# Optimization experiments

Hardware: AMD Instinct MI355X
Metric: run time of the kernel (lower is better)

## Reference

```python
import jax, jax.numpy as jnp
import numpy as np

P_SCALAR = 40.0
NEG_INF = -1e9


def setup_inputs() -> dict:
    key = jax.random.key(0)
    ks = jax.random.split(key, 6)
    B, Dk, Dv, T, H, W = 2, 128, 512, 2, 64, 64
    qkey = jax.random.normal(ks[0], (B, Dk, H, W), dtype=jnp.float32)
    qval = jax.random.normal(ks[1], (B, Dv, H, W), dtype=jnp.float32)
    mkey = jax.random.normal(ks[2], (B, Dk, T, H, W), dtype=jnp.float32)
    mval = jax.random.normal(ks[3], (B, Dv, T, H, W), dtype=jnp.float32)
    qmask = jax.random.bernoulli(ks[4], 0.5, (B, 1, H, W))
    mmask = jax.random.bernoulli(ks[5], 0.5, (B, 1, T, H, W))
    return {"qkey": qkey, "qval": qval, "qmask": qmask,
            "mkey": mkey, "mval": mval, "mmask": mmask}


def reference(qkey, qval, qmask, mkey, mval, mmask):
    # Faithful vectorized version of maskRead: for each batch, attention from
    # masked query pixels over masked memory pixels, scatter back into zeros.
    # Boolean-gather + softmax over gathered rows == full softmax with masked
    # logits set to -inf (rows outside mmask get zero probability).
    B, Dk, H, W = qkey.shape
    Dv = qval.shape[1]
    qk = qkey.reshape(B, Dk, H * W)            # [B, Dk, Nq]
    mk = mkey.reshape(B, Dk, -1)               # [B, Dk, Nm]
    mv = mval.reshape(B, Dv, -1)               # [B, Dv, Nm]
    qm = qmask.reshape(B, H * W)               # [B, Nq]
    mm = mmask.reshape(B, -1)                  # [B, Nm]

    # p[b, m, q] = <mk[b,:,m], qk[b,:,q]> * p_scalar, softmax over m
    p = jnp.einsum('bdm,bdq->bmq', mk, qk) * P_SCALAR
    p = jnp.where(mm[:, :, None], p, NEG_INF)
    p = jax.nn.softmax(p, axis=1)              # [B, Nm, Nq]

    read = jnp.einsum('bvm,bmq->bvq', mv, p)   # [B, Dv, Nq]

    # zero out query pixels outside qmask; skip batches with empty masks
    valid = qm[:, None, :] & mm.any(axis=1)[:, None, None] & qm.any(axis=1)[:, None, None]
    qread = jnp.where(valid, read, 0.0)
    return qread.reshape(B, Dv, H, W)
```

## Files before the change

kernel.cpp:

```cpp
#include <hip/hip_runtime.h>

#define NQ 4096
#define NM 8192
#define DK 128
#define DV 512
#define BATCH 2
#define NT (NM / 64)
#define KTS 8192
#define VTILE 16384

typedef __attribute__((ext_vector_type(8))) short short8;
typedef __attribute__((ext_vector_type(4))) float f32x4;
typedef unsigned short ushort_t;

#define MF(A_, B_, C_) __builtin_amdgcn_mfma_f32_16x16x32_bf16(A_, B_, C_, 0, 0, 0)

static __device__ __forceinline__ unsigned short f2bf(float x) {
    union { float f; unsigned int u; } c; c.f = x;
    unsigned int u = c.u;
    return (unsigned short)((u + 0x7FFFu + ((u >> 16) & 1u)) >> 16);
}
static __device__ __forceinline__ float bf2f(unsigned short h) {
    union { unsigned int u; float f; } c; c.u = ((unsigned int)h) << 16;
    return c.f;
}

static __device__ __forceinline__ size_t vaddr(int b, int pos, int dv) {
    const int mt = pos >> 6, m64 = pos & 63;
    const int dvh = dv >> 8, rr = dv & 255;
    return (((size_t)(b * NT + mt) * 2 + dvh) * VTILE)
         + (rr >> 6) * 4096 + ((rr >> 4) & 3) * 1024
         + (m64 >> 5) * 512
         + ((((m64 >> 4) & 1) * 2 + ((m64 >> 3) & 1)) * 128)
         + (rr & 15) * 8 + (m64 & 7);
}

#define LOADK(AH, AL, itn_) do {                                              \
    const size_t ktb_ = kbase + (size_t)(itn_) * KTS;                         \
    _Pragma("unroll")                                                         \
    for (int ks_ = 0; ks_ < 4; ++ks_) {                                       \
        AH[ks_] = *(const short8*)(kh0 + ktb_ + ks_ * 512);                   \
        AL[ks_] = *(const short8*)(kl0 + ktb_ + ks_ * 512);                   \
    }                                                                         \
} while (0)

__global__ __launch_bounds__(1024) void scan_kernel(
    const int* __restrict__ qmask, const int* __restrict__ mmask,
    int* __restrict__ cidx, int* __restrict__ cpos,
    int* __restrict__ cnts, int* __restrict__ qflags) {
    const int b = blockIdx.x;
    const int t = threadIdx.x;
    const int lane = t & 63;
    const int w = t >> 6;
    __shared__ int wsum[16];
    __shared__ int qsh;

    const int* mp = mmask + b * NM;
    const int base = t * 8;
    int val[8];
#pragma unroll
    for (int i = 0; i < 8; ++i) val[i] = (mp[base + i] != 0);
    int c0 = 0;
#pragma unroll
    for (int i = 0; i < 8; ++i) c0 += val[i];

    int c = c0;
#pragma unroll
    for (int off = 1; off < 64; off <<= 1) {
        int n = __shfl_up(c, off, 64);
        if (lane >= off) c += n;
    }
    if (lane == 63) wsum[w] = c;
    if (t == 0) qsh = 0;
    __syncthreads();
    if (t == 0) {
        int s = 0;
#pragma unroll
        for (int i = 0; i < 16; ++i) { s += wsum[i]; wsum[i] = s; }
    }
    __syncthreads();
    const int wbase = (w == 0) ? 0 : wsum[w - 1];
    int run = wbase + (c - c0);
#pragma unroll
    for (int i = 0; i < 8; ++i) {
        int m = base + i;
        cpos[b * NM + m] = run;
        if (val[i]) { cidx[b * NM + run] = m; ++run; }
    }

    int qa = 0;
    for (int i = t; i < NQ; i += 1024) qa |= (qmask[b * NQ + i] != 0);
    if (qa) atomicOr(&qsh, 1);
    __syncthreads();
    if (t == 0) { cnts[b] = wsum[15]; qflags[b] = qsh; }
}

__global__ __launch_bounds__(256) void prep_all_kernel(
    const float* __restrict__ qkey, const float* __restrict__ mkey,
    const float* __restrict__ mval, const int* __restrict__ mmask,
    const int* __restrict__ cpos, const int* __restrict__ cnts,
    ushort_t* __restrict__ Qhi, ushort_t* __restrict__ Qlo,
    ushort_t* __restrict__ Khi, ushort_t* __restrict__ Klo,
    ushort_t* __restrict__ Vc) {
    __shared__ float t32[32][33];
    const int g = blockIdx.x;

    if (g < 1024) {
        const int bx = g & 127, by = (g >> 7) & 3, b = g >> 9;
        const int d0 = by * 32, n0 = bx * 32;
        for (int l = threadIdx.x; l < 1024; l += 256) {
            int r = l >> 5, c = l & 31;
            t32[r][c] = qkey[((size_t)b * DK + d0 + r) * NQ + n0 + c];
        }
        __syncthreads();
        for (int l = threadIdx.x; l < 1024; l += 256) {
            int r = l >> 5, c = l & 31;
            float f = t32[c][r];
            unsigned short h = f2bf(f);
            unsigned short lw = f2bf(f - bf2f(h));
            size_t off = ((size_t)b * NQ + n0 + r) * DK + d0 + c;
            Qhi[off] = h;
            Qlo[off] = lw;
        }
        return;
    }
    if (g < 3072) {
        const int h0 = g - 1024;
        const int bx = h0 & 255, by = (h0 >> 8) & 3, b = h0 >> 10;
        const int d0 = by * 32, n0 = bx * 32;
        for (int l = threadIdx.x; l < 1024; l += 256) {
            int r = l >> 5, c = l & 31;
            t32[r][c] = mkey[((size_t)b * DK + d0 + r) * NM + n0 + c];
        }
        __syncthreads();
        for (int l = threadIdx.x; l < 1024; l += 256) {
            int r = l >> 5, c = l & 31;
            int m = n0 + r;
            if (mmask[b * NM + m] != 0) {
                int pos = cpos[b * NM + m];
                float f = t32[c][r];
                unsigned short hh = f2bf(f);
                unsigned short lw = f2bf(f - bf2f(hh));
                int d = d0 + c;
                size_t off = ((size_t)(b * NT + (pos >> 6))) * KTS
                           + ((pos >> 4) & 3) * 2048 + (d >> 5) * 512
                           + ((d >> 3) & 3) * 128 + (pos & 15) * 8 + (d & 7);
                Khi[off] = hh;
                Klo[off] = lw;
            }
        }
        return;
    }
    const int h0 = g - 3072;
    const int bx = h0 & 63;
    const int by = (h0 >> 6) % 9;
    const int b = h0 / 576;
    const int dv0 = bx * 8;
    if (by == 8) {
        const int cnt = cnts[b];
        const int pend = ((cnt + 63) >> 6) * 64;
        const int dv = dv0 + (threadIdx.x >> 5);
        for (int p = cnt + (threadIdx.x & 31); p < pend; p += 32)
            Vc[vaddr(b, p, dv)] = 0;
        return;
    }
    const int m = by * 1024 + threadIdx.x * 4;
    const int4 mm = *(const int4*)(mmask + b * NM + m);
    const int4 cp = *(const int4*)(cpos + b * NM + m);
#pragma unroll
    for (int i = 0; i < 8; ++i) {
        const int dv = dv0 + i;
        const float4 v = *(const float4*)(mval + ((size_t)b * DV + dv) * NM + m);
        if (mm.x) Vc[vaddr(b, cp.x, dv)] = f2bf(v.x);
        if (mm.y) Vc[vaddr(b, cp.y, dv)] = f2bf(v.y);
        if (mm.z) Vc[vaddr(b, cp.z, dv)] = f2bf(v.z);
        if (mm.w) Vc[vaddr(b, cp.w, dv)] = f2bf(v.w);
    }
}

__global__ __launch_bounds__(256, 3) void stats_kernel(
    const ushort_t* __restrict__ Qhi, const ushort_t* __restrict__ Khi,
    const int* __restrict__ cnts, float* __restrict__ mpart) {
    const int t = threadIdx.x;
    const int lane = t & 63;
    const int w = t >> 6;
    const int quad = lane >> 4;
    const int col = lane & 15;
    const int bid = blockIdx.x;
    const int part = bid & 3;
    const int b = (bid >> 2) & 1;
    const int qb = (bid >> 3) * 64;

    const int cnt = cnts[b];
    const int nit = (cnt + 63) >> 6;
    const int it0 = (nit * part) >> 2;
    const int it1 = (nit * (part + 1)) >> 2;

    __shared__ float red_m[4][64];

    short8 qfh[4][4];
    {
        const ushort_t* qhp = Qhi + ((size_t)b * NQ + qb) * DK;
#pragma unroll
        for (int qt = 0; qt < 4; ++qt)
#pragma unroll
            for (int ks = 0; ks < 4; ++ks)
                qfh[qt][ks] = *(const short8*)(qhp + (size_t)(qt * 16 + col) * DK + ks * 32 + quad * 8);
    }

    const f32x4 zero4 = {0.f, 0.f, 0.f, 0.f};
    float mloc[4] = {-3.0e38f, -3.0e38f, -3.0e38f, -3.0e38f};
    const ushort_t* kh0 = Khi + w * 2048 + lane * 8;
    const size_t kbase = (size_t)(b * NT) * KTS;

#define LOADKH(A_, itn_) do {                                                 \
    const size_t ktb_ = kbase + (size_t)(itn_) * KTS;                         \
    _Pragma("unroll")                                                         \
    for (int ks_ = 0; ks_ < 4; ++ks_)                                         \
        A_[ks_] = *(const short8*)(kh0 + ktb_ + ks_ * 512);                   \
} while (0)

#define STPH(CK, NK, it_, itn_) do {                                          \
    LOADKH(NK, itn_);                                                         \
    f32x4 aS[4];                                                              \
    _Pragma("unroll")                                                         \
    for (int qt = 0; qt < 4; ++qt) aS[qt] = zero4;                            \
    _Pragma("unroll")                                                         \
    for (int ks = 0; ks < 4; ++ks)                                            \
        _Pragma("unroll")                                                     \
        for (int qt = 0; qt < 4; ++qt)                                        \
            aS[qt] = MF(CK[ks], qfh[qt][ks], aS[qt]);                         \
    const int mrow_ = (it_) * 64 + w * 16 + quad * 4;                         \
    _Pragma("unroll")                                                         \
    for (int r = 0; r < 4; ++r) {                                             \
        if (mrow_ + r < cnt) {                                                \
            _Pragma("unroll")                                                 \
            for (int qt = 0; qt < 4; ++qt)                                    \
                mloc[qt] = fmaxf(mloc[qt], aS[qt][r] * 40.0f);                \
        }                                                                     \
    }                                                                         \
} while (0)

    short8 kA[4], kB[4];
    int it = it0;
    if (it < it1) {
        LOADKH(kA, it);
        int itn;
        while (true) {
            itn = (it + 1 < it1) ? it + 1 : it;
            STPH(kA, kB, it, itn);
            if (++it >= it1) break;
            itn = (it + 1 < it1) ? it + 1 : it;
            STPH(kB, kA, it, itn);
            if (++it >= it1) break;
        }
    }
#undef STPH
#undef LOADKH

#pragma unroll
    for (int qt = 0; qt < 4; ++qt) {
        float m = mloc[qt];
        m = fmaxf(m, __shfl_xor(m, 16, 64));
        m = fmaxf(m, __shfl_xor(m, 32, 64));
        if (lane < 16) red_m[w][qt * 16 + col] = m;
    }
    __syncthreads();
    if (t < 64) {
        float M = -3.0e38f;
#pragma unroll
        for (int ww = 0; ww < 4; ++ww) M = fmaxf(M, red_m[ww][t]);
        mpart[((size_t)(b * 4 + part)) * NQ + qb + t] = M;
    }
}

__global__ __launch_bounds__(256, 3) void pv_kernel(
    const ushort_t* __restrict__ Qhi, const ushort_t* __restrict__ Qlo,
    const ushort_t* __restrict__ Khi, const ushort_t* __restrict__ Klo,
    const ushort_t* __restrict__ Vimg, const int* __restrict__ cnts,
    const float* __restrict__ mpart, float* __restrict__ out0,
    float* __restrict__ out1, float* __restrict__ out2,
    float* __restrict__ lsum) {
    const int t = threadIdx.x;
    const int lane = t & 63;
    const int w = t >> 6;
    const int quad = lane >> 4;
    const int col = lane & 15;
    const int bid = blockIdx.x;
    const int b = bid & 1;
    const int dvh = (bid >> 1) & 1;
    const int r3 = bid >> 2;
    const int chunk = r3 % 3;
    const int qb = (r3 / 3) * 64;

    const int cnt = cnts[b];
    const int nit = (cnt + 63) >> 6;
    const int it0 = (nit * chunk) / 3;
    const int it1 = (nit * (chunk + 1)) / 3;

    __shared__ __align__(16) ushort_t Q_s[2][4][4][512];
    __shared__ __align__(16) ushort_t P_s[2][64][68];

    float gm[4];
#pragma unroll
    for (int qt = 0; qt < 4; ++qt) {
        float M = -3.0e38f;
#pragma unroll
        for (int c = 0; c < 4; ++c)
            M = fmaxf(M, mpart[((size_t)(b * 4 + c)) * NQ + qb + qt * 16 + col]);
        gm[qt] = M + 8.0f;
    }

    {
        const int r = t >> 2, ks4 = t & 3;
        const int qt_ = r >> 4, col_ = r & 15;
        const ushort_t* qhp = Qhi + ((size_t)b * NQ + qb + r) * DK + ks4 * 32;
        const ushort_t* qlp = Qlo + ((size_t)b * NQ + qb + r) * DK + ks4 * 32;
#pragma unroll
        for (int qd = 0; qd < 4; ++qd) {
            *(short8*)&Q_s[0][qt_][ks4][qd * 128 + col_ * 8] = *(const short8*)(qhp + qd * 8);
            *(short8*)&Q_s[1][qt_][ks4][qd * 128 + col_ * 8] = *(const short8*)(qlp + qd * 8);
        }
    }
    __syncthreads();

    const ushort_t* kh0 = Khi + w * 2048 + lane * 8;
    const ushort_t* kl0 = Klo + w * 2048 + lane * 8;
    const size_t kbase = (size_t)(b * NT) * KTS;
    const ushort_t* vl0 = Vimg + ((size_t)(b * NT) * 2 + dvh) * VTILE
                        + w * 4096 + lane * 8;

    const f32x4 zero4 = {0.f, 0.f, 0.f, 0.f};
    const short8 vones = {(short)0x3F80, (short)0x3F80, (short)0x3F80,
                          (short)0x3F80, (short)0x3F80, (short)0x3F80,
                          (short)0x3F80, (short)0x3F80};
    const bool doL = (dvh == 0) && (w == 0);
    f32x4 accO[4][4];
#pragma unroll
    for (int vt = 0; vt < 4; ++vt)
#pragma unroll
        for (int qt = 0; qt < 4; ++qt) accO[vt][qt] = zero4;
    f32x4 accL[4];
#pragma unroll
    for (int qt = 0; qt < 4; ++qt) accL[qt] = zero4;

    for (int it = it0; it < it1; ++it) {
        const int pb = (it - it0) & 1;
        short8 kh[4], kl[4];
        LOADK(kh, kl, it);
        f32x4 aS[4];
#pragma unroll
        for (int qt = 0; qt < 4; ++qt) aS[qt] = zero4;
#pragma unroll
        for (int qt = 0; qt < 4; ++qt) {
#pragma unroll
            for (int ks = 0; ks < 4; ++ks) {
                const short8 qh = *(const short8*)&Q_s[0][qt][ks][lane * 8];
                const short8 ql = *(const short8*)&Q_s[1][qt][ks][lane * 8];
                aS[qt] = MF(kh[ks], qh, aS[qt]);
                aS[qt] = MF(kh[ks], ql, aS[qt]);
                aS[qt] = MF(kl[ks], qh, aS[qt]);
            }
        }
        const ushort_t* vp = vl0 + (size_t)it * (2 * VTILE);
        short8 vf[4][2];
#pragma unroll
        for (int vt = 0; vt < 4; ++vt) {
            vf[vt][0] = *(const short8*)(vp + vt * 1024);
            vf[vt][1] = *(const short8*)(vp + vt * 1024 + 512);
        }
        const int mrow = it * 64 + w * 16 + quad * 4;
#pragma unroll
        for (int qt = 0; qt < 4; ++qt) {
            float p[4];
#pragma unroll
            for (int r = 0; r < 4; ++r)
                p[r] = (mrow + r < cnt) ? __expf(aS[qt][r] * 40.0f - gm[qt]) : 0.0f;
            ushort4 pk;
            pk.x = f2bf(p[0]); pk.y = f2bf(p[1]);
            pk.z = f2bf(p[2]); pk.w = f2bf(p[3]);
            *(ushort4*)&P_s[pb][qt * 16 + col][w * 16 + quad * 4] = pk;
        }
        asm volatile("s_waitcnt lgkmcnt(0)" ::: "memory");
        __builtin_amdgcn_s_barrier();
        __builtin_amdgcn_sched_barrier(0);
#pragma unroll
        for (int k2 = 0; k2 < 2; ++k2) {
            short8 pq[4];
#pragma unroll
            for (int qt = 0; qt < 4; ++qt)
                pq[qt] = *(const short8*)&P_s[pb][qt * 16 + col][k2 * 32 + quad * 8];
#pragma unroll
            for (int vt = 0; vt < 4; ++vt)
#pragma unroll
                for (int qt = 0; qt < 4; ++qt)
                    accO[vt][qt] = MF(vf[vt][k2], pq[qt], accO[vt][qt]);
            if (doL) {
#pragma unroll
                for (int qt = 0; qt < 4; ++qt)
                    accL[qt] = MF(vones, pq[qt], accL[qt]);
            }
        }
    }

    float* pbase = (chunk == 0) ? out0 : ((chunk == 1) ? out1 : out2);
#pragma unroll
    for (int qt = 0; qt < 4; ++qt) {
        const int q = qb + qt * 16 + col;
#pragma unroll
        for (int vt = 0; vt < 4; ++vt)
#pragma unroll
            for (int r = 0; r < 4; ++r) {
                int dv = dvh * 256 + w * 64 + vt * 16 + quad * 4 + r;
                pbase[((size_t)b * DV + dv) * NQ + q] = accO[vt][qt][r];
            }
    }
    if (doL && lane < 16) {
#pragma unroll
        for (int qt = 0; qt < 4; ++qt)
            lsum[((size_t)(b * 3 + chunk)) * NQ + qb + qt * 16 + col] = accL[qt][0];
    }
}

__global__ __launch_bounds__(256) void combine_kernel(
    const float* p0, const float* __restrict__ p1,
    const float* __restrict__ p2, const float* __restrict__ lsum,
    const int* __restrict__ cnts, const int* __restrict__ qflags,
    const int* __restrict__ qmask, float* out) {
    const size_t i = ((size_t)blockIdx.x * 256 + threadIdx.x) * 4;
    const int b = (int)(i >> 21);
    const int q = (int)(i & (NQ - 1));
    f32x4 a = *(const f32x4*)(p0 + i);
    f32x4 c = *(const f32x4*)(p1 + i);
    f32x4 d = *(const f32x4*)(p2 + i);
    f32x4 l0 = *(const f32x4*)(lsum + (size_t)(b * 3) * NQ + q);
    f32x4 l1 = *(const f32x4*)(lsum + (size_t)(b * 3 + 1) * NQ + q);
    f32x4 l2 = *(const f32x4*)(lsum + (size_t)(b * 3 + 2) * NQ + q);
    const int4 qm = *(const int4*)(qmask + b * NQ + q);
    const bool bv = (qflags[b] != 0) && (cnts[b] > 0);
    f32x4 r;
    float lv;
    lv = l0[0] + l1[0] + l2[0]; r[0] = (bv && qm.x && lv > 0.f) ? (a[0] + c[0] + d[0]) / lv : 0.f;
    lv = l0[1] + l1[1] + l2[1]; r[1] = (bv && qm.y && lv > 0.f) ? (a[1] + c[1] + d[1]) / lv : 0.f;
    lv = l0[2] + l1[2] + l2[2]; r[2] = (bv && qm.z && lv > 0.f) ? (a[2] + c[2] + d[2]) / lv : 0.f;
    lv = l0[3] + l1[3] + l2[3]; r[3] = (bv && qm.w && lv > 0.f) ? (a[3] + c[3] + d[3]) / lv : 0.f;
    *(f32x4*)(out + i) = r;
}

extern "C" void kernel_launch(void* const* d_in, const int* in_sizes, int n_in,
                              void* d_out, int out_size, void* d_ws, size_t ws_size,
                              hipStream_t stream) {
    const float* qkey  = (const float*)d_in[0];
    const int*   qmask = (const int*)d_in[2];
    const float* mkey  = (const float*)d_in[3];
    const float* mval  = (const float*)d_in[4];
    const int*   mmask = (const int*)d_in[5];
    float* out = (float*)d_out;

    char* ws = (char*)d_ws;
    size_t off = 0;
    const size_t QS  = (size_t)BATCH * NQ * DK * 2;
    const size_t KS2 = (size_t)BATCH * NM * DK * 2;
    const size_t VS  = (size_t)BATCH * NT * 2 * VTILE * 2;
    const size_t OS  = (size_t)BATCH * DV * NQ * 4;
    ushort_t* Qhi = (ushort_t*)(ws + off); off += QS;
    ushort_t* Qlo = (ushort_t*)(ws + off); off += QS;
    ushort_t* Khi = (ushort_t*)(ws + off); off += KS2;
    ushort_t* Klo = (ushort_t*)(ws + off); off += KS2;
    ushort_t* Vc  = (ushort_t*)(ws + off); off += VS;
    float* part1  = (float*)(ws + off); off += OS;
    float* part2  = (float*)(ws + off); off += OS;
    float* mpart  = (float*)(ws + off); off += (size_t)BATCH * 4 * NQ * 4;
    float* lsum   = (float*)(ws + off); off += (size_t)BATCH * 3 * NQ * 4;
    int* cidx     = (int*)(ws + off); off += (size_t)BATCH * NM * 4;
    int* cpos     = (int*)(ws + off); off += (size_t)BATCH * NM * 4;
    int* cnts     = (int*)(ws + off); off += 64;
    int* qflags   = (int*)(ws + off); off += 64;

    scan_kernel<<<BATCH, 1024, 0, stream>>>(qmask, mmask, cidx, cpos, cnts, qflags);

    prep_all_kernel<<<4224, 256, 0, stream>>>(
        qkey, mkey, mval, mmask, cpos, cnts, Qhi, Qlo, Khi, Klo, Vc);

    stats_kernel<<<(NQ / 64) * 8, 256, 0, stream>>>(Qhi, Khi, cnts, mpart);

    pv_kernel<<<(NQ / 64) * 12, 256, 0, stream>>>(
        Qhi, Qlo, Khi, Klo, Vc, cnts, mpart, out, part1, part2, lsum);

    combine_kernel<<<(int)((size_t)BATCH * DV * NQ / 1024), 256, 0, stream>>>(
        out, part1, part2, lsum, cnts, qflags, qmask, out);
}
```

Before: 233.9 us.

## Store split-K partial outputs in fp16, split prep kernel, add MFMA priority hints

The three split-K partial output buffers are now stored as fp16 instead of fp32, and all three go to the workspace instead of one aliasing the output. This halves the partial-result write and read traffic between pv_kernel and combine_kernel. The prep kernel is split into a Q/K conversion kernel and a separate V compaction kernel with a 3D grid. s_setprio is raised around the MFMA loops in pv_kernel. Rounding unnormalized partial sums to fp16 adds precision error and could overflow if the partial sums exceed the fp16 range.

Measured after the change: 221.6 us. 1.06x faster.

```diff
diff --git a/kernel.cpp b/kernel.cpp
--- a/kernel.cpp
+++ b/kernel.cpp
@@ -1,4 +1,5 @@
 #include <hip/hip_runtime.h>
+#include <hip/hip_fp16.h>
 
 #define NQ 4096
 #define NM 8192
@@ -23,6 +24,14 @@
 static __device__ __forceinline__ float bf2f(unsigned short h) {
     union { unsigned int u; float f; } c; c.u = ((unsigned int)h) << 16;
     return c.f;
+}
+static __device__ __forceinline__ ushort_t f2h(float x) {
+    __half h = __float2half(x);
+    return *(ushort_t*)&h;
+}
+static __device__ __forceinline__ float h2f(ushort_t u) {
+    __half h = *(__half*)&u;
+    return __half2float(h);
 }
 
 static __device__ __forceinline__ size_t vaddr(int b, int pos, int dv) {
@@ -95,13 +104,11 @@
     if (t == 0) { cnts[b] = wsum[15]; qflags[b] = qsh; }
 }
 
-__global__ __launch_bounds__(256) void prep_all_kernel(
+__global__ __launch_bounds__(256) void prep_qk_kernel(
     const float* __restrict__ qkey, const float* __restrict__ mkey,
-    const float* __restrict__ mval, const int* __restrict__ mmask,
-    const int* __restrict__ cpos, const int* __restrict__ cnts,
+    const int* __restrict__ mmask, const int* __restrict__ cpos,
     ushort_t* __restrict__ Qhi, ushort_t* __restrict__ Qlo,
-    ushort_t* __restrict__ Khi, ushort_t* __restrict__ Klo,
-    ushort_t* __restrict__ Vc) {
+    ushort_t* __restrict__ Khi, ushort_t* __restrict__ Klo) {
     __shared__ float t32[32][33];
     const int g = blockIdx.x;
 
@@ -124,57 +131,57 @@
         }
         return;
     }
-    if (g < 3072) {
-        const int h0 = g - 1024;
-        const int bx = h0 & 255, by = (h0 >> 8) & 3, b = h0 >> 10;
-        const int d0 = by * 32, n0 = bx * 32;
-        for (int l = threadIdx.x; l < 1024; l += 256) {
-            int r = l >> 5, c = l & 31;
-            t32[r][c] = mkey[((size_t)b * DK + d0 + r) * NM + n0 + c];
-        }
-        __syncthreads();
-        for (int l = threadIdx.x; l < 1024; l += 256) {
-            int r = l >> 5, c = l & 31;
-            int m = n0 + r;
-            if (mmask[b * NM + m] != 0) {
-                int pos = cpos[b * NM + m];
-                float f = t32[c][r];
-                unsigned short hh = f2bf(f);
-                unsigned short lw = f2bf(f - bf2f(hh));
-                int d = d0 + c;
-                size_t off = ((size_t)(b * NT + (pos >> 6))) * KTS
-                           + ((pos >> 4) & 3) * 2048 + (d >> 5) * 512
-                           + ((d >> 3) & 3) * 128 + (pos & 15) * 8 + (d & 7);
-                Khi[off] = hh;
-                Klo[off] = lw;
-            }
-        }
-        return;
-    }
-    const int h0 = g - 3072;
-    const int bx = h0 & 63;
-    const int by = (h0 >> 6) % 9;
-    const int b = h0 / 576;
-    const int dv0 = bx * 8;
-    if (by == 8) {
+    const int h0 = g - 1024;
+    const int bx = h0 & 255, by = (h0 >> 8) & 3, b = h0 >> 10;
+    const int d0 = by * 32, n0 = bx * 32;
+    for (int l = threadIdx.x; l < 1024; l += 256) {
+        int r = l >> 5, c = l & 31;
+        t32[r][c] = mkey[((size_t)b * DK + d0 + r) * NM + n0 + c];
+    }
+    __syncthreads();
+    for (int l = threadIdx.x; l < 1024; l += 256) {
+        int r = l >> 5, c = l & 31;
+        int m = n0 + r;
+        if (mmask[b * NM + m] != 0) {
+            int pos = cpos[b * NM + m];
+            float f = t32[c][r];
+            unsigned short hh = f2bf(f);
+            unsigned short lw = f2bf(f - bf2f(hh));
+            int d = d0 + c;
+            size_t off = ((size_t)(b * NT + (pos >> 6))) * KTS
+                       + ((pos >> 4) & 3) * 2048 + (d >> 5) * 512
+                       + ((d >> 3) & 3) * 128 + (pos & 15) * 8 + (d & 7);
+            Khi[off] = hh;
+            Klo[off] = lw;
+        }
+    }
+}
+
+__global__ __launch_bounds__(256) void prep_v_kernel(
+    const float* __restrict__ src, const int* __restrict__ mmask,
+    const int* __restrict__ cpos, const int* __restrict__ cnts,
+    ushort_t* __restrict__ dst) {
+    const int b = blockIdx.z;
+    const int dv0 = blockIdx.x * 8;
+    if (blockIdx.y == 8) {
         const int cnt = cnts[b];
         const int pend = ((cnt + 63) >> 6) * 64;
         const int dv = dv0 + (threadIdx.x >> 5);
         for (int p = cnt + (threadIdx.x & 31); p < pend; p += 32)
-            Vc[vaddr(b, p, dv)] = 0;
+            dst[vaddr(b, p, dv)] = 0;
         return;
     }
-    const int m = by * 1024 + threadIdx.x * 4;
+    const int m = blockIdx.y * 1024 + threadIdx.x * 4;
     const int4 mm = *(const int4*)(mmask + b * NM + m);
     const int4 cp = *(const int4*)(cpos + b * NM + m);
 #pragma unroll
     for (int i = 0; i < 8; ++i) {
         const int dv = dv0 + i;
-        const float4 v = *(const float4*)(mval + ((size_t)b * DV + dv) * NM + m);
-        if (mm.x) Vc[vaddr(b, cp.x, dv)] = f2bf(v.x);
-        if (mm.y) Vc[vaddr(b, cp.y, dv)] = f2bf(v.y);
-        if (mm.z) Vc[vaddr(b, cp.z, dv)] = f2bf(v.z);
-        if (mm.w) Vc[vaddr(b, cp.w, dv)] = f2bf(v.w);
+        const float4 v = *(const float4*)(src + ((size_t)b * DV + dv) * NM + m);
+        if (mm.x) dst[vaddr(b, cp.x, dv)] = f2bf(v.x);
+        if (mm.y) dst[vaddr(b, cp.y, dv)] = f2bf(v.y);
+        if (mm.z) dst[vaddr(b, cp.z, dv)] = f2bf(v.z);
+        if (mm.w) dst[vaddr(b, cp.w, dv)] = f2bf(v.w);
     }
 }
 
@@ -278,8 +285,8 @@
     const ushort_t* __restrict__ Qhi, const ushort_t* __restrict__ Qlo,
     const ushort_t* __restrict__ Khi, const ushort_t* __restrict__ Klo,
     const ushort_t* __restrict__ Vimg, const int* __restrict__ cnts,
-    const float* __restrict__ mpart, float* __restrict__ out0,
-    float* __restrict__ out1, float* __restrict__ out2,
+    const float* __restrict__ mpart, ushort_t* __restrict__ out0,
+    ushort_t* __restrict__ out1, ushort_t* __restrict__ out2,
     float* __restrict__ lsum) {
     const int t = threadIdx.x;
     const int lane = t & 63;
@@ -351,6 +358,7 @@
         f32x4 aS[4];
 #pragma unroll
         for (int qt = 0; qt < 4; ++qt) aS[qt] = zero4;
+        __builtin_amdgcn_s_setprio(1);
 #pragma unroll
         for (int qt = 0; qt < 4; ++qt) {
 #pragma unroll
@@ -362,6 +370,7 @@
                 aS[qt] = MF(kl[ks], qh, aS[qt]);
             }
         }
+        __builtin_amdgcn_s_setprio(0);
         const ushort_t* vp = vl0 + (size_t)it * (2 * VTILE);
         short8 vf[4][2];
 #pragma unroll
@@ -384,6 +393,7 @@
         asm volatile("s_waitcnt lgkmcnt(0)" ::: "memory");
         __builtin_amdgcn_s_barrier();
         __builtin_amdgcn_sched_barrier(0);
+        __builtin_amdgcn_s_setprio(1);
 #pragma unroll
         for (int k2 = 0; k2 < 2; ++k2) {
             short8 pq[4];
@@ -401,9 +411,10 @@
                     accL[qt] = MF(vones, pq[qt], accL[qt]);
             }
         }
-    }
-
-    float* pbase = (chunk == 0) ? out0 : ((chunk == 1) ? out1 : out2);
+        __builtin_amdgcn_s_setprio(0);
+    }
+
+    ushort_t* pbase = (chunk == 0) ? out0 : ((chunk == 1) ? out1 : out2);
 #pragma unroll
     for (int qt = 0; qt < 4; ++qt) {
         const int q = qb + qt * 16 + col;
@@ -412,7 +423,7 @@
 #pragma unroll
             for (int r = 0; r < 4; ++r) {
                 int dv = dvh * 256 + w * 64 + vt * 16 + quad * 4 + r;
-                pbase[((size_t)b * DV + dv) * NQ + q] = accO[vt][qt][r];
+                pbase[((size_t)b * DV + dv) * NQ + q] = f2h(accO[vt][qt][r]);
             }
     }
     if (doL && lane < 16) {
@@ -423,16 +434,16 @@
 }
 
 __global__ __launch_bounds__(256) void combine_kernel(
-    const float* p0, const float* __restrict__ p1,
-    const float* __restrict__ p2, const float* __restrict__ lsum,
+    const ushort_t* __restrict__ p0, const ushort_t* __restrict__ p1,
+    const ushort_t* __restrict__ p2, const float* __restrict__ lsum,
     const int* __restrict__ cnts, const int* __restrict__ qflags,
-    const int* __restrict__ qmask, float* out) {
+    const int* __restrict__ qmask, float* __restrict__ out) {
     const size_t i = ((size_t)blockIdx.x * 256 + threadIdx.x) * 4;
     const int b = (int)(i >> 21);
     const int q = (int)(i & (NQ - 1));
-    f32x4 a = *(const f32x4*)(p0 + i);
-    f32x4 c = *(const f32x4*)(p1 + i);
-    f32x4 d = *(const f32x4*)(p2 + i);
+    ushort4 a4 = *(const ushort4*)(p0 + i);
+    ushort4 c4 = *(const ushort4*)(p1 + i);
+    ushort4 d4 = *(const ushort4*)(p2 + i);
     f32x4 l0 = *(const f32x4*)(lsum + (size_t)(b * 3) * NQ + q);
     f32x4 l1 = *(const f32x4*)(lsum + (size_t)(b * 3 + 1) * NQ + q);
     f32x4 l2 = *(const f32x4*)(lsum + (size_t)(b * 3 + 2) * NQ + q);
@@ -440,10 +451,14 @@
     const bool bv = (qflags[b] != 0) && (cnts[b] > 0);
     f32x4 r;
     float lv;
-    lv = l0[0] + l1[0] + l2[0]; r[0] = (bv && qm.x && lv > 0.f) ? (a[0] + c[0] + d[0]) / lv : 0.f;
-    lv = l0[1] + l1[1] + l2[1]; r[1] = (bv && qm.y && lv > 0.f) ? (a[1] + c[1] + d[1]) / lv : 0.f;
-    lv = l0[2] + l1[2] + l2[2]; r[2] = (bv && qm.z && lv > 0.f) ? (a[2] + c[2] + d[2]) / lv : 0.f;
-    lv = l0[3] + l1[3] + l2[3]; r[3] = (bv && qm.w && lv > 0.f) ? (a[3] + c[3] + d[3]) / lv : 0.f;
+    lv = l0[0] + l1[0] + l2[0];
+    r[0] = (bv && qm.x && lv > 0.f) ? (h2f(a4.x) + h2f(c4.x) + h2f(d4.x)) / lv : 0.f;
+    lv = l0[1] + l1[1] + l2[1];
+    r[1] = (bv && qm.y && lv > 0.f) ? (h2f(a4.y) + h2f(c4.y) + h2f(d4.y)) / lv : 0.f;
+    lv = l0[2] + l1[2] + l2[2];
+    r[2] = (bv && qm.z && lv > 0.f) ? (h2f(a4.z) + h2f(c4.z) + h2f(d4.z)) / lv : 0.f;
+    lv = l0[3] + l1[3] + l2[3];
+    r[3] = (bv && qm.w && lv > 0.f) ? (h2f(a4.w) + h2f(c4.w) + h2f(d4.w)) / lv : 0.f;
     *(f32x4*)(out + i) = r;
 }
 
@@ -462,14 +477,15 @@
     const size_t QS  = (size_t)BATCH * NQ * DK * 2;
     const size_t KS2 = (size_t)BATCH * NM * DK * 2;
     const size_t VS  = (size_t)BATCH * NT * 2 * VTILE * 2;
-    const size_t OS  = (size_t)BATCH * DV * NQ * 4;
+    const size_t OS2 = (size_t)BATCH * DV * NQ * 2;
     ushort_t* Qhi = (ushort_t*)(ws + off); off += QS;
     ushort_t* Qlo = (ushort_t*)(ws + off); off += QS;
     ushort_t* Khi = (ushort_t*)(ws + off); off += KS2;
     ushort_t* Klo = (ushort_t*)(ws + off); off += KS2;
     ushort_t* Vc  = (ushort_t*)(ws + off); off += VS;
-    float* part1  = (float*)(ws + off); off += OS;
-    float* part2  = (float*)(ws + off); off += OS;
+    ushort_t* part0 = (ushort_t*)(ws + off); off += OS2;
+    ushort_t* part1 = (ushort_t*)(ws + off); off += OS2;
+    ushort_t* part2 = (ushort_t*)(ws + off); off += OS2;
     float* mpart  = (float*)(ws + off); off += (size_t)BATCH * 4 * NQ * 4;
     float* lsum   = (float*)(ws + off); off += (size_t)BATCH * 3 * NQ * 4;
     int* cidx     = (int*)(ws + off); off += (size_t)BATCH * NM * 4;
@@ -479,14 +495,17 @@
 
     scan_kernel<<<BATCH, 1024, 0, stream>>>(qmask, mmask, cidx, cpos, cnts, qflags);
 
-    prep_all_kernel<<<4224, 256, 0, stream>>>(
-        qkey, mkey, mval, mmask, cpos, cnts, Qhi, Qlo, Khi, Klo, Vc);
+    prep_qk_kernel<<<3072, 256, 0, stream>>>(
+        qkey, mkey, mmask, cpos, Qhi, Qlo, Khi, Klo);
+
+    dim3 gv(DV / 8, 9, BATCH);
+    prep_v_kernel<<<gv, 256, 0, stream>>>(mval, mmask, cpos, cnts, Vc);
 
     stats_kernel<<<(NQ / 64) * 8, 256, 0, stream>>>(Qhi, Khi, cnts, mpart);
 
     pv_kernel<<<(NQ / 64) * 12, 256, 0, stream>>>(
-        Qhi, Qlo, Khi, Klo, Vc, cnts, mpart, out, part1, part2, lsum);
+        Qhi, Qlo, Khi, Klo, Vc, cnts, mpart, part0, part1, part2, lsum);
 
     combine_kernel<<<(int)((size_t)BATCH * DV * NQ / 1024), 256, 0, stream>>>(
-        out, part1, part2, lsum, cnts, qflags, qmask, out);
-}
+        part0, part1, part2, lsum, cnts, qflags, qmask, out);
+}
```
